# Performance work log

Measured on AMD Instinct MI355X. Metric: run time of the kernel, lower is better.

## Reference

```python
import jax, jax.numpy as jnp
import numpy as np

NUM_RELATIONS = 3
NUM_HEADS = 1

N_NODES = 50000
N_EDGES = 300000
D = 256  # in_channels == out_channels == out_channels*num_heads
W_SCALE = 0.02  # realistic init scale; keeps linear-attention normalizer dominated by N_r


def setup_inputs() -> dict:
    key = jax.random.key(0)
    k = jax.random.split(key, 7)
    x = jax.random.normal(k[0], (N_NODES, D), dtype=jnp.float32)
    Wq = jax.random.normal(k[1], (NUM_RELATIONS, D, D * NUM_HEADS), dtype=jnp.float32) * W_SCALE
    Wk = jax.random.normal(k[2], (NUM_RELATIONS, D, D * NUM_HEADS), dtype=jnp.float32) * W_SCALE
    Wv = jax.random.normal(k[3], (NUM_RELATIONS, D, D * NUM_HEADS), dtype=jnp.float32) * W_SCALE
    Whp = jax.random.normal(k[4], (D * NUM_HEADS, D), dtype=jnp.float32) * W_SCALE
    edge_index = jax.random.randint(k[5], (2, N_EDGES), 0, N_NODES, dtype=jnp.int64)
    edge_type = jax.random.randint(k[6], (N_EDGES,), 0, NUM_RELATIONS, dtype=jnp.int64)
    return {"x": x, "Wq": Wq, "Wk": Wk, "Wv": Wv, "Whp": Whp,
            "edge_index": edge_index, "edge_type": edge_type}


def _trans_conv(x, Wq, Wk, Wv, Whp, edge_index, edge_type):
    # x: [N, F], Wq/Wk/Wv: [R, F, H*Dh], Whp: [H*Dh, Dh], edge_index: [2, E]
    row, col = edge_index[0], edge_index[1]
    N = x.shape[0]
    R = Wq.shape[0]
    H = NUM_HEADS
    Dh = Wq.shape[-1] // H
    xr = x[row]  # [E, F] gathered source-node features
    xc = x[col]  # [E, F] gathered target-node features
    x_out = jnp.zeros((N, Dh), dtype=x.dtype)
    for r in range(R):  # small fixed relation loop (structurally distinct weights)
        m = (edge_type == r).astype(x.dtype)  # [E] relation mask (handles ragged sizes)
        Nr = jnp.sum(m)  # number of edges of this relation (the 'N' in full_attention_conv)
        q = (xr @ Wq[r]).reshape(-1, H, Dh)  # [E, H, Dh]
        kk = (xc @ Wk[r]).reshape(-1, H, Dh)
        v = (xc @ Wv[r]).reshape(-1, H, Dh)
        # linear attention (no softmax), masked so only relation-r edges contribute
        kvs = jnp.einsum('e,ehm,ehd->hmd', m, kk, v)        # [H, Dh, Dh]
        num = jnp.einsum('ehm,hmd->ehd', q, kvs) + Nr * v    # [E, H, Dh]
        ks_sum = jnp.einsum('e,ehm->hm', m, kk)              # [H, Dh]
        norm = jnp.einsum('ehm,hm->eh', q, ks_sum)[..., None] + Nr  # [E, H, 1]
        attn = (num / norm).mean(axis=1)                     # [E, Dh] (mean over heads)
        x_out = x_out.at[row].add(m[:, None] * attn)         # scatter-add to source nodes
    return x_out @ Whp  # head projection


def reference(x, Wq, Wk, Wv, Whp, edge_index, edge_type):
    return _trans_conv(x, Wq, Wk, Wv, Whp, edge_index, edge_type)
```

## Files before the change

### kernel.cpp

```cpp
#include <hip/hip_runtime.h>

#define NN 50000
#define EE 300000
#define DD 256
#define RR 3
#define NPAD 50048
#define GS 64
#define SCT (RR * NN)
#define SCB 1024
#define SNB ((SCT + SCB - 1) / SCB)
#define TBLK 3128
#define WBLK 2560
#define CBLK 512

using bf16x8 = __attribute__((ext_vector_type(8))) short;
using f32x4  = __attribute__((ext_vector_type(4))) float;

__device__ __forceinline__ float bf2f(unsigned short u) {
    return __uint_as_float(((unsigned)u) << 16);
}
__device__ __forceinline__ unsigned short f2bf(float f) {
    unsigned u = __float_as_uint(f);
    return (unsigned short)((u + 0x7fffu + ((u >> 16) & 1u)) >> 16);
}
__device__ __forceinline__ void gload_lds16(const void* g, void* l) {
    __builtin_amdgcn_global_load_lds(
        (const __attribute__((address_space(1))) unsigned int*)g,
        (__attribute__((address_space(3))) unsigned int*)l, 16, 0, 0);
}

__global__ __launch_bounds__(256) void prep_tc(
    const float* __restrict__ x, const float* __restrict__ Wq,
    const float* __restrict__ Wk, const float* __restrict__ Wv,
    const float* __restrict__ Whp,
    unsigned short* __restrict__ xb, unsigned short* __restrict__ xT,
    unsigned short* __restrict__ Wqb, unsigned short* __restrict__ Wkb,
    unsigned short* __restrict__ Wvb, unsigned short* __restrict__ WhpT,
    const int* __restrict__ erow, const int* __restrict__ ecol,
    const int* __restrict__ etype, int* __restrict__ c_in,
    int* __restrict__ c_out, int* __restrict__ nr)
{
    const int tid = threadIdx.x;
    if (blockIdx.x < TBLK) {
        __shared__ unsigned short t[64][66];
        const int tb = blockIdx.x;
        const int n0 = (tb % 782) * 64, i0 = (tb / 782) * 64;
        const int nl = tid >> 2, c0 = (tid & 3) * 16;
        unsigned short vb[16];
        int n = n0 + nl;
        if (n < NN) {
            const float* src = x + (size_t)n * DD + i0 + c0;
#pragma unroll
            for (int q = 0; q < 16; q += 4) {
                float4 v = *(const float4*)(src + q);
                vb[q] = f2bf(v.x); vb[q + 1] = f2bf(v.y);
                vb[q + 2] = f2bf(v.z); vb[q + 3] = f2bf(v.w);
            }
#pragma unroll
            for (int q = 0; q < 16; q += 4)
                *(ushort4*)(xb + (size_t)n * DD + i0 + c0 + q) =
                    make_ushort4(vb[q], vb[q + 1], vb[q + 2], vb[q + 3]);
        } else {
#pragma unroll
            for (int q = 0; q < 16; q++) vb[q] = 0;
        }
#pragma unroll
        for (int q = 0; q < 16; q++) t[nl][c0 + q] = vb[q];
        __syncthreads();
        const int il = tid >> 2, nc0 = (tid & 3) * 16;
        unsigned short ob[16];
#pragma unroll
        for (int q = 0; q < 16; q++) ob[q] = t[nc0 + q][il];
#pragma unroll
        for (int q = 0; q < 16; q += 4)
            *(ushort4*)(xT + (size_t)(i0 + il) * NPAD + n0 + nc0 + q) =
                make_ushort4(ob[q], ob[q + 1], ob[q + 2], ob[q + 3]);
    } else if (blockIdx.x < TBLK + WBLK) {
        int t = (blockIdx.x - TBLK) * 256 + tid;
        int slot = t >> 16, o = t & 65535;
        int a = o >> 8, b = o & 255;
        if (slot < 3)       Wqb[(size_t)slot * 65536 + o] = f2bf(Wq[(size_t)slot * 65536 + o]);
        else if (slot < 6)  Wkb[(size_t)(slot - 3) * 65536 + o] = f2bf(Wk[(size_t)(slot - 3) * 65536 + o]);
        else if (slot < 9)  Wvb[(size_t)(slot - 6) * 65536 + o] = f2bf(Wv[(size_t)(slot - 6) * 65536 + o]);
        else if (slot == 9) WhpT[o] = f2bf(Whp[b * 256 + a]);
    } else {
        __shared__ int lnr[RR];
        if (tid < RR) lnr[tid] = 0;
        __syncthreads();
        int cb = blockIdx.x - (TBLK + WBLK);
        for (int e = cb * 256 + tid; e < EE; e += CBLK * 256) {
            int t = etype[e];
            atomicAdd(&c_out[t * NN + erow[e]], 1);
            atomicAdd(&c_in[t * NN + ecol[e]], 1);
            atomicAdd(&lnr[t], 1);
        }
        __syncthreads();
        if (tid < RR) atomicAdd(&nr[tid], lnr[tid]);
    }
}

__global__ __launch_bounds__(256) void prep2(
    const int* __restrict__ c_out, int* __restrict__ bsum,
    const unsigned short* __restrict__ xT, const int* __restrict__ c_in,
    float* __restrict__ xw, unsigned short* __restrict__ wbf)
{
    const int tid = threadIdx.x;
    if (blockIdx.x < SNB) {
        __shared__ int ws[4];
        const int b = blockIdx.x;
        const int i = b * SCB + tid * 4;
        int s = 0;
        if (i < SCT) {
            int4 v = *(const int4*)(c_out + i);
            s = v.x + v.y + v.z + v.w;
        }
#pragma unroll
        for (int off = 32; off; off >>= 1) s += __shfl_down(s, off, 64);
        if ((tid & 63) == 0) ws[tid >> 6] = s;
        __syncthreads();
        if (tid == 0) bsum[b] = ws[0] + ws[1] + ws[2] + ws[3];
    } else if (blockIdx.x < SNB + 256) {
        __shared__ float red[3][4];
        const int i = blockIdx.x - SNB;
        float a0 = 0.f, a1 = 0.f, a2 = 0.f;
        for (int n = tid * 4; n < NN; n += 1024) {
            ushort4 xv = *(const ushort4*)(xT + (size_t)i * NPAD + n);
            int4 w0 = *(const int4*)(c_in + n);
            int4 w1 = *(const int4*)(c_in + NN + n);
            int4 w2 = *(const int4*)(c_in + 2 * NN + n);
            float f0 = bf2f(xv.x), f1 = bf2f(xv.y), f2 = bf2f(xv.z), f3 = bf2f(xv.w);
            a0 += f0 * w0.x + f1 * w0.y + f2 * w0.z + f3 * w0.w;
            a1 += f0 * w1.x + f1 * w1.y + f2 * w1.z + f3 * w1.w;
            a2 += f0 * w2.x + f1 * w2.y + f2 * w2.z + f3 * w2.w;
        }
#pragma unroll
        for (int off = 32; off; off >>= 1) {
            a0 += __shfl_down(a0, off, 64);
            a1 += __shfl_down(a1, off, 64);
            a2 += __shfl_down(a2, off, 64);
        }
        if ((tid & 63) == 0) {
            red[0][tid >> 6] = a0; red[1][tid >> 6] = a1; red[2][tid >> 6] = a2;
        }
        __syncthreads();
        if (tid < 3)
            xw[tid * 256 + i] = red[tid][0] + red[tid][1] + red[tid][2] + red[tid][3];
    } else {
        int t = (blockIdx.x - SNB - 256) * 256 + tid;
        if (t < 3 * NPAD) {
            int r = t / NPAD, n = t % NPAD;
            wbf[t] = f2bf(n < NN ? (float)c_in[r * NN + n] : 0.f);
        }
    }
}

__global__ __launch_bounds__(256) void scan_bot(
    const int* __restrict__ cnt, const int* __restrict__ bsum,
    int* __restrict__ off, int* __restrict__ cur)
{
    __shared__ int bs[256], loc[256];
    const int b = blockIdx.x, tid = threadIdx.x;
    int v = tid < SNB ? bsum[tid] : 0;
    bs[tid] = v;
    __syncthreads();
    for (int d = 1; d < 256; d <<= 1) {
        int t = (tid >= d) ? bs[tid - d] : 0;
        __syncthreads();
        bs[tid] += t;
        __syncthreads();
    }
    const int myboff = b ? bs[b - 1] : 0;
    const int total = bs[255];
    const int i = b * SCB + tid * 4;
    int4 vv = make_int4(0, 0, 0, 0);
    if (i < SCT) vv = *(const int4*)(cnt + i);
    int s = vv.x + vv.y + vv.z + vv.w;
    loc[tid] = s;
    __syncthreads();
    for (int d = 1; d < 256; d <<= 1) {
        int t = (tid >= d) ? loc[tid - d] : 0;
        __syncthreads();
        loc[tid] += t;
        __syncthreads();
    }
    if (i < SCT) {
        int pre = myboff + (tid ? loc[tid - 1] : 0);
        int4 o;
        o.x = pre;
        o.y = pre + vv.x;
        o.z = pre + vv.x + vv.y;
        o.w = pre + vv.x + vv.y + vv.z;
        *(int4*)(off + i) = o;
        *(int4*)(cur + i) = o;
    }
    if (b == 0 && tid == 0) off[SCT] = total;
}

__global__ __launch_bounds__(256) void fill_kernel(
    const int* __restrict__ erow, const int* __restrict__ ecol,
    const int* __restrict__ etype, int* __restrict__ cur,
    int* __restrict__ scol)
{
    int e = blockIdx.x * 256 + threadIdx.x;
    if (e < EE) {
        int key = etype[e] * NN + erow[e];
        int p = atomicAdd(&cur[key], 1);
        scol[p] = ecol[e];
    }
}

__global__ __launch_bounds__(512) void g_kernel(
    const unsigned short* __restrict__ xT, const unsigned short* __restrict__ wbf,
    float* __restrict__ Gp)
{
    __shared__ __align__(16) char ldsA[16384];
    __shared__ __align__(16) char ldsB[16384];
    const int tid = threadIdx.x, lane = tid & 63, wid = tid >> 6;
    const int wr = wid >> 1, wc = wid & 1;
    const int i0 = blockIdx.x * 128, j0 = blockIdx.y * 128;
    const int TPZ = (NPAD / 64 + GS - 1) / GS;
    const int kt0 = blockIdx.z * TPZ;
    const int kt1 = min(NPAD / 64, kt0 + TPZ);

    f32x4 acc[3][2][4];
#pragma unroll
    for (int r = 0; r < 3; r++)
#pragma unroll
        for (int m = 0; m < 2; m++)
#pragma unroll
            for (int n = 0; n < 4; n++) acc[r][m][n] = (f32x4){0.f, 0.f, 0.f, 0.f};

    for (int kt = kt0; kt < kt1; kt++) {
        const int kbyte = kt * 128;
#pragma unroll
        for (int is = 0; is < 2; is++) {
            int lb = is * 8192 + wid * 1024;
            int d = lb + lane * 16;
            int row = d >> 7;
            int sc_ = (d & 127) ^ ((row & 7) << 4);
            gload_lds16((const char*)xT + (size_t)(i0 + row) * (NPAD * 2) + kbyte + sc_, ldsA + lb);
            gload_lds16((const char*)xT + (size_t)(j0 + row) * (NPAD * 2) + kbyte + sc_, ldsB + lb);
        }
        __syncthreads();
#pragma unroll
        for (int kk = 0; kk < 2; kk++) {
            const int cb = kk * 64 + ((lane >> 4) << 4);
            bf16x8 bfr[4];
#pragma unroll
            for (int n = 0; n < 4; n++) {
                int rn = wc * 64 + n * 16 + (lane & 15);
                bfr[n] = *(const bf16x8*)(ldsB + rn * 128 + (cb ^ ((rn & 7) << 4)));
            }
            float au[2][8];
#pragma unroll
            for (int m = 0; m < 2; m++) {
                int row = wr * 32 + m * 16 + (lane & 15);
                bf16x8 ar = *(const bf16x8*)(ldsA + row * 128 + (cb ^ ((row & 7) << 4)));
#pragma unroll
                for (int q = 0; q < 8; q++) au[m][q] = bf2f((unsigned short)ar[q]);
            }
            const int nb = kt * 64 + kk * 32 + ((lane >> 4) << 3);
#pragma unroll
            for (int r = 0; r < 3; r++) {
                bf16x8 wv = *(const bf16x8*)(wbf + (size_t)r * NPAD + nb);
                float wf[8];
#pragma unroll
                for (int q = 0; q < 8; q++) wf[q] = bf2f((unsigned short)wv[q]);
                bf16x8 am[2];
#pragma unroll
                for (int m = 0; m < 2; m++)
#pragma unroll
                    for (int q = 0; q < 8; q++)
                        am[m][q] = (short)f2bf(au[m][q] * wf[q]);
#pragma unroll
                for (int m = 0; m < 2; m++)
#pragma unroll
                    for (int n = 0; n < 4; n++)
                        acc[r][m][n] = __builtin_amdgcn_mfma_f32_16x16x32_bf16(
                            am[m], bfr[n], acc[r][m][n], 0, 0, 0);
            }
        }
        __syncthreads();
    }
    float* base = Gp + ((size_t)blockIdx.z * 4 + blockIdx.x * 2 + blockIdx.y) * 3 * 16384;
#pragma unroll
    for (int r = 0; r < 3; r++)
#pragma unroll
        for (int m = 0; m < 2; m++)
#pragma unroll
            for (int n = 0; n < 4; n++) {
                int col = wc * 64 + n * 16 + (lane & 15);
                int rw0 = wr * 32 + m * 16 + ((lane >> 4) << 2);
#pragma unroll
                for (int reg = 0; reg < 4; reg++)
                    base[r * 16384 + (rw0 + reg) * 128 + col] = acc[r][m][n][reg];
            }
}

__global__ __launch_bounds__(256) void gred_mv(
    const float* __restrict__ Gp, unsigned short* __restrict__ Gb,
    const unsigned short* __restrict__ M1, const float* __restrict__ xw,
    float* __restrict__ tv)
{
    const int tid = threadIdx.x;
    if (blockIdx.x < 768) {
        int gid = blockIdx.x * 256 + tid;
        int t = gid >> 14, rem = gid & 16383;
        int r = t % 3, tile = t / 3;
        float s = 0.f;
        for (int z = 0; z < GS; z++)
            s += Gp[(size_t)z * 196608 + ((size_t)tile * 3 + r) * 16384 + rem];
        int i = (tile >> 1) * 128 + (rem >> 7);
        int j = (tile & 1) * 128 + (rem & 127);
        Gb[(size_t)r * 65536 + i * 256 + j] = f2bf(s);
    } else {
        __shared__ float vs[256];
        const int b = blockIdx.x - 768;
        const int r = b >> 6, rb = (b & 63) * 4;
        vs[tid] = xw[r * 256 + tid];
        __syncthreads();
        const int wid = tid >> 6, lane = tid & 63;
        const int row = rb + wid;
        ushort4 m4 = *(const ushort4*)(M1 + (size_t)r * 65536 + row * 256 + lane * 4);
        float s = bf2f(m4.x) * vs[lane * 4] + bf2f(m4.y) * vs[lane * 4 + 1] +
                  bf2f(m4.z) * vs[lane * 4 + 2] + bf2f(m4.w) * vs[lane * 4 + 3];
#pragma unroll
        for (int off = 32; off; off >>= 1) s += __shfl_down(s, off, 64);
        if (lane == 0) tv[r * 256 + row] = s;
    }
}

__global__ __launch_bounds__(256) void gather_kernel(
    const unsigned short* __restrict__ xb, const int* __restrict__ scol,
    const int* __restrict__ off, const float* __restrict__ tv,
    const int* __restrict__ c_out, const int* __restrict__ nr,
    unsigned short* __restrict__ Ascat, float* __restrict__ s2g)
{
    __shared__ float ts[768];
    __shared__ float nrs[RR];
    const int tid = threadIdx.x;
    for (int k = tid; k < 768; k += 256) ts[k] = tv[k];
    if (tid < RR) nrs[tid] = (float)nr[tid];
    __syncthreads();
    const int wid = tid >> 6, lane = tid & 63;
    const int n = blockIdx.x * 4 + wid;
    if (n >= NN) return;
    ushort4 xv = *(const ushort4*)(xb + (size_t)n * DD + lane * 4);
    float xf[4] = {bf2f(xv.x), bf2f(xv.y), bf2f(xv.z), bf2f(xv.w)};
    float dots[RR];
#pragma unroll
    for (int t = 0; t < RR; t++) {
        float s = xf[0] * ts[t * 256 + lane * 4] + xf[1] * ts[t * 256 + lane * 4 + 1] +
                  xf[2] * ts[t * 256 + lane * 4 + 2] + xf[3] * ts[t * 256 + lane * 4 + 3];
#pragma unroll
        for (int o = 32; o; o >>= 1) s += __shfl_xor(s, o, 64);
        dots[t] = s;
    }
    int i0 = off[0 * NN + n], e0 = off[0 * NN + n + 1];
    int i1 = off[1 * NN + n], e1 = off[1 * NN + n + 1];
    int i2 = off[2 * NN + n], e2 = off[2 * NN + n + 1];
    float a0[4] = {0.f, 0.f, 0.f, 0.f};
    float a1[4] = {0.f, 0.f, 0.f, 0.f};
    float a2[4] = {0.f, 0.f, 0.f, 0.f};
    while (i0 < e0 || i1 < e1 || i2 < e2) {
        bool h0 = i0 < e0, h1 = i1 < e1, h2 = i2 < e2;
        ushort4 v0, v1, v2;
        if (h0) { int c = scol[i0]; v0 = *(const ushort4*)(xb + (size_t)c * DD + lane * 4); }
        if (h1) { int c = scol[i1]; v1 = *(const ushort4*)(xb + (size_t)c * DD + lane * 4); }
        if (h2) { int c = scol[i2]; v2 = *(const ushort4*)(xb + (size_t)c * DD + lane * 4); }
        if (h0) { a0[0] += bf2f(v0.x); a0[1] += bf2f(v0.y);
                  a0[2] += bf2f(v0.z); a0[3] += bf2f(v0.w); i0++; }
        if (h1) { a1[0] += bf2f(v1.x); a1[1] += bf2f(v1.y);
                  a1[2] += bf2f(v1.z); a1[3] += bf2f(v1.w); i1++; }
        if (h2) { a2[0] += bf2f(v2.x); a2[1] += bf2f(v2.y);
                  a2[2] += bf2f(v2.z); a2[3] += bf2f(v2.w); i2++; }
    }
    float* accs[3] = {a0, a1, a2};
#pragma unroll
    for (int t = 0; t < RR; t++) {
        float nrf = nrs[t];
        float denom = dots[t] + nrf;
        if (lane == 0) {
            int cnt = c_out[t * NN + n];
            s2g[(size_t)t * NN + n] = cnt ? (float)cnt / denom : 0.f;
        }
        float s1 = nrf / denom;
        float* a = accs[t];
        ushort4 o2;
        o2.x = f2bf(s1 * a[0]); o2.y = f2bf(s1 * a[1]);
        o2.z = f2bf(s1 * a[2]); o2.w = f2bf(s1 * a[3]);
        *(ushort4*)(Ascat + (size_t)n * 768 + t * 256 + lane * 4) = o2;
    }
}

template <int MODE, int SWZ>
__global__ __launch_bounds__(256) void gemm_nt(
    const unsigned short* __restrict__ A, int lda,
    const unsigned short* __restrict__ B, int ldb,
    void* __restrict__ Cv, int ldc, int M, int KK,
    size_t sa, size_t sb, size_t sc)
{
    A += (size_t)blockIdx.z * sa;
    B += (size_t)blockIdx.z * sb;
    __shared__ __align__(16) char ldsA[16384];
    __shared__ __align__(16) char ldsB[16384];
    const int tid = threadIdx.x, lane = tid & 63, wid = tid >> 6;
    const int wr = wid >> 1, wc = wid & 1;
    int bx = blockIdx.x;
    if (SWZ) {
        int nwg = gridDim.x, q = nwg >> 3, rem = nwg & 7;
        int xcd = bx & 7, idx = bx >> 3;
        bx = (xcd < rem ? xcd * (q + 1) : rem * (q + 1) + (xcd - rem) * q) + idx;
    }
    const int row0 = bx * 128, col0 = blockIdx.y * 128;

    f32x4 acc[4][4];
#pragma unroll
    for (int m = 0; m < 4; m++)
#pragma unroll
        for (int n = 0; n < 4; n++) acc[m][n] = (f32x4){0.f, 0.f, 0.f, 0.f};

    for (int k0 = 0; k0 < KK; k0 += 64) {
#pragma unroll
        for (int is = 0; is < 4; is++) {
            int lb = is * 4096 + wid * 1024;
            int d = lb + lane * 16;
            int row = d >> 7;
            int sc_ = (d & 127) ^ ((row & 7) << 4);
            int gr = row0 + row; gr = gr < M ? gr : M - 1;
            gload_lds16((const char*)(A + (size_t)gr * lda + k0) + sc_, ldsA + lb);
            int rn = col0 + row;
            gload_lds16((const char*)(B + (size_t)rn * ldb + k0) + sc_, ldsB + lb);
        }
        __syncthreads();
#pragma unroll
        for (int kk = 0; kk < 2; kk++) {
            bf16x8 af[4], bf_[4];
            const int cb = kk * 64 + ((lane >> 4) << 4);
#pragma unroll
            for (int m = 0; m < 4; m++) {
                int row = wr * 64 + m * 16 + (lane & 15);
                af[m] = *(const bf16x8*)(ldsA + row * 128 + (cb ^ ((row & 7) << 4)));
                int rn = wc * 64 + m * 16 + (lane & 15);
                bf_[m] = *(const bf16x8*)(ldsB + rn * 128 + (cb ^ ((rn & 7) << 4)));
            }
#pragma unroll
            for (int m = 0; m < 4; m++)
#pragma unroll
                for (int n = 0; n < 4; n++)
                    acc[m][n] = __builtin_amdgcn_mfma_f32_16x16x32_bf16(
                        af[m], bf_[n], acc[m][n], 0, 0, 0);
        }
        __syncthreads();
    }

#pragma unroll
    for (int m = 0; m < 4; m++) {
#pragma unroll
        for (int reg = 0; reg < 4; reg++) {
            int r = row0 + wr * 64 + m * 16 + ((lane >> 4) << 2) + reg;
            if (r >= M) continue;
#pragma unroll
            for (int n = 0; n < 4; n++) {
                int c = col0 + wc * 64 + n * 16 + (lane & 15);
                float v = acc[m][n][reg];
                if (MODE == 0)
                    ((unsigned short*)Cv)[(size_t)blockIdx.z * sc + (size_t)r * ldc + c] = f2bf(v);
                else
                    ((float*)Cv)[(size_t)blockIdx.z * sc + (size_t)r * ldc + c] = v;
            }
        }
    }
}

__global__ __launch_bounds__(512) void gemm_big(
    const unsigned short* __restrict__ Xb, const unsigned short* __restrict__ As,
    const unsigned short* __restrict__ Bm, const float* __restrict__ s2g,
    float* __restrict__ C, int M)
{
    extern __shared__ __align__(16) char lds[];
    char* ldsA = lds;
    char* ldsB = lds + 32768;
    float* s2l = (float*)(lds + 98304);
    const int tid = threadIdx.x, lane = tid & 63, wid = tid >> 6;
    const int wr = wid >> 2, wc = wid & 3;
    int bx = blockIdx.x;
    {
        int nwg = gridDim.x, q = nwg >> 3, rem = nwg & 7;
        int xcd = bx & 7, idx = bx >> 3;
        bx = (xcd < rem ? xcd * (q + 1) : rem * (q + 1) + (xcd - rem) * q) + idx;
    }
    const int row0 = bx * 128;

    if (tid < 384) {
        int rsel = tid >> 7, rr = tid & 127;
        int gr = row0 + rr; gr = gr < M ? gr : M - 1;
        s2l[tid] = s2g[(size_t)rsel * NN + gr];
    }

    f32x4 accO[4][4], acc[4][4];
#pragma unroll
    for (int m = 0; m < 4; m++)
#pragma unroll
        for (int n = 0; n < 4; n++) {
            accO[m][n] = (f32x4){0.f, 0.f, 0.f, 0.f};
            acc[m][n]  = (f32x4){0.f, 0.f, 0.f, 0.f};
        }

#define STAGE_A(buf, Asrc, ldaE, kE)                                           \
    { _Pragma("unroll")                                                        \
      for (int is = 0; is < 2; is++) {                                         \
          int lb = is * 8192 + wid * 1024;                                     \
          int d = lb + lane * 16;                                              \
          int row = d >> 7;                                                    \
          int sc_ = (d & 127) ^ ((row & 7) << 4);                              \
          int gr = row0 + row; gr = gr < M ? gr : M - 1;                       \
          gload_lds16((const char*)((Asrc) + (size_t)gr * (ldaE) + (kE)) + sc_,\
                      ldsA + (buf) * 16384 + lb); } }

#define STAGE_B(buf, kE)                                                       \
    { _Pragma("unroll")                                                        \
      for (int is = 0; is < 4; is++) {                                         \
          int lb = is * 8192 + wid * 1024;                                     \
          int d = lb + lane * 16;                                              \
          int row = d >> 7;                                                    \
          int sc_ = (d & 127) ^ ((row & 7) << 4);                              \
          gload_lds16((const char*)(Bm + (size_t)row * 1536 + (kE)) + sc_,     \
                      ldsB + (buf) * 32768 + lb); } }

#define MFMA_STEP(abuf, bbuf, ACC)                                             \
    { const char* bA = ldsA + (abuf) * 16384;                                  \
      const char* bB = ldsB + (bbuf) * 32768;                                  \
      _Pragma("unroll")                                                        \
      for (int kk = 0; kk < 2; kk++) {                                         \
          bf16x8 af[4], bf_[4];                                                \
          const int cb = kk * 64 + ((lane >> 4) << 4);                         \
          _Pragma("unroll")                                                    \
          for (int m = 0; m < 4; m++) {                                        \
              int row = wr * 64 + m * 16 + (lane & 15);                        \
              af[m] = *(const bf16x8*)(bA + row * 128 + (cb ^ ((row & 7) << 4)));\
              int rn = wc * 64 + m * 16 + (lane & 15);                         \
              bf_[m] = *(const bf16x8*)(bB + rn * 128 + (cb ^ ((rn & 7) << 4)));\
          }                                                                    \
          _Pragma("unroll")                                                    \
          for (int m = 0; m < 4; m++)                                          \
              _Pragma("unroll")                                                \
              for (int n = 0; n < 4; n++)                                      \
                  ACC[m][n] = __builtin_amdgcn_mfma_f32_16x16x32_bf16(         \
                      af[m], bf_[n], ACC[m][n], 0, 0, 0); } }

    STAGE_A(0, Xb, 256, 0);
    STAGE_B(0, 0);
    __syncthreads();
    int ab = 0, bb = 0;

    for (int r = 0; r < 3; r++) {
        for (int kt = 0; kt < 4; kt++) {
            if (kt < 3)      { STAGE_A(ab ^ 1, Xb, 256, (kt + 1) * 64);
                               STAGE_B(bb ^ 1, r * 256 + (kt + 1) * 64); }
            else if (r < 2)  { STAGE_A(ab ^ 1, Xb, 256, 0);
                               STAGE_B(bb ^ 1, (r + 1) * 256); }
            else             { STAGE_A(ab ^ 1, As, 768, 0);
                               STAGE_B(bb ^ 1, 768); }
            MFMA_STEP(ab, bb, acc);
            __syncthreads();
            ab ^= 1; bb ^= 1;
        }
#pragma unroll
        for (int m = 0; m < 4; m++) {
            f32x4 sv = *(const f32x4*)&s2l[r * 128 + wr * 64 + m * 16 + ((lane >> 4) << 2)];
#pragma unroll
            for (int n = 0; n < 4; n++) {
                accO[m][n] += sv * acc[m][n];
                acc[m][n] = (f32x4){0.f, 0.f, 0.f, 0.f};
            }
        }
    }
    for (int st = 0; st < 12; st++) {
        if (st < 11) { STAGE_A(ab ^ 1, As, 768, (st + 1) * 64);
                       STAGE_B(bb ^ 1, 768 + (st + 1) * 64); }
        MFMA_STEP(ab, bb, accO);
        __syncthreads();
        ab ^= 1; bb ^= 1;
    }
#undef STAGE_A
#undef STAGE_B
#undef MFMA_STEP

#pragma unroll
    for (int m = 0; m < 4; m++) {
#pragma unroll
        for (int reg = 0; reg < 4; reg++) {
            int r = row0 + wr * 64 + m * 16 + ((lane >> 4) << 2) + reg;
            if (r >= M) continue;
#pragma unroll
            for (int n = 0; n < 4; n++) {
                int c = wc * 64 + n * 16 + (lane & 15);
                C[(size_t)r * 256 + c] = accO[m][n][reg];
            }
        }
    }
}

extern "C" void kernel_launch(void* const* d_in, const int* in_sizes, int n_in,
                              void* d_out, int out_size, void* d_ws, size_t ws_size,
                              hipStream_t stream)
{
    const float* x   = (const float*)d_in[0];
    const float* Wq  = (const float*)d_in[1];
    const float* Wk  = (const float*)d_in[2];
    const float* Wv  = (const float*)d_in[3];
    const float* Whp = (const float*)d_in[4];
    const int* eidx  = (const int*)d_in[5];
    const int* etyp  = (const int*)d_in[6];
    const int* erow = eidx;
    const int* ecol = eidx + EE;
    float* out = (float*)d_out;

    char* p = (char*)d_ws;
    unsigned short* xb    = (unsigned short*)p; p += (size_t)NN * DD * 2;
    unsigned short* xT    = (unsigned short*)p; p += (size_t)DD * NPAD * 2;
    char*           regB  = p;                  p += (size_t)NN * 768 * 2;
    unsigned short* Gb    = (unsigned short*)p; p += (size_t)RR * 65536 * 2;
    unsigned short* M1    = (unsigned short*)p; p += (size_t)RR * 65536 * 2;
    unsigned short* Tm    = (unsigned short*)p; p += (size_t)RR * 65536 * 2;
    unsigned short* Bout  = (unsigned short*)p; p += (size_t)256 * 1536 * 2;
    unsigned short* Wqb   = (unsigned short*)p; p += (size_t)RR * 65536 * 2;
    unsigned short* Wkb   = (unsigned short*)p; p += (size_t)RR * 65536 * 2;
    unsigned short* Wvb   = (unsigned short*)p; p += (size_t)RR * 65536 * 2;
    unsigned short* WhpT  = (unsigned short*)p; p += 65536 * 2;
    unsigned short* wbf   = (unsigned short*)p; p += (size_t)RR * NPAD * 2;
    float*          xw    = (float*)p;          p += 768 * 4;
    float*          tv    = (float*)p;          p += 768 * 4;
    float*          s2g   = (float*)p;          p += (size_t)RR * NN * 4;
    int*            c_in  = (int*)p;            p += (size_t)RR * NN * 4;
    int*            c_out = (int*)p;            p += (size_t)RR * NN * 4;
    int*            nr    = (int*)p;            p += 4 * 4;
    int*            off   = (int*)p;            p += (size_t)(RR * NN + 4) * 4;
    int*            cur   = (int*)p;            p += (size_t)RR * NN * 4;
    int*            scol  = (int*)p;            p += (size_t)EE * 4;
    int*            bsum  = (int*)p;            p += SNB * 4;
    float*          Gp    = (float*)regB;
    unsigned short* Ascat = (unsigned short*)regB;

    hipFuncSetAttribute((const void*)gemm_big,
                        hipFuncAttributeMaxDynamicSharedMemorySize, 99840);

    hipMemsetAsync(c_in, 0, (size_t)(6 * NN + 4) * sizeof(int), stream);
    prep_tc<<<TBLK + WBLK + CBLK, 256, 0, stream>>>(
        x, Wq, Wk, Wv, Whp, xb, xT, Wqb, Wkb, Wvb, WhpT,
        erow, ecol, etyp, c_in, c_out, nr);
    prep2<<<SNB + 256 + (3 * NPAD + 255) / 256, 256, 0, stream>>>(
        c_out, bsum, xT, c_in, xw, wbf);
    scan_bot<<<SNB, 256, 0, stream>>>(c_out, bsum, off, cur);
    fill_kernel<<<(EE + 255) / 256, 256, 0, stream>>>(erow, ecol, etyp, cur, scol);

    gemm_nt<0, 0><<<dim3(2, 2, 3), 256, 0, stream>>>(Wqb, 256, Wkb, 256, M1, 256, 256, 256,
                                                     65536, 65536, 65536);
    gemm_nt<0, 0><<<dim3(2, 2, 3), 256, 0, stream>>>(WhpT, 256, Wvb, 256, Bout + 768, 1536,
                                                     256, 256, 0, 65536, 256);

    g_kernel<<<dim3(2, 2, GS), 512, 0, stream>>>(xT, wbf, Gp);
    gred_mv<<<768 + 192, 256, 0, stream>>>(Gp, Gb, M1, xw, tv);

    gemm_nt<0, 0><<<dim3(2, 2, 3), 256, 0, stream>>>(M1, 256, Gb, 256, Tm, 256, 256, 256,
                                                     65536, 65536, 65536);
    gemm_nt<0, 0><<<dim3(2, 2, 3), 256, 0, stream>>>(Bout + 768, 1536, Tm, 256, Bout, 1536,
                                                     256, 256, 256, 65536, 256);

    gather_kernel<<<(NN + 3) / 4, 256, 0, stream>>>(
        xb, scol, off, tv, c_out, nr, Ascat, s2g);

    const int MB2 = (NN + 127) / 128;
    gemm_big<<<dim3(MB2, 1), 512, 99840, stream>>>(xb, Ascat, Bout, s2g, out, NN);
}
```

Measured before the change: 289.3 us.

## Triple-buffer gemm_big LDS with two-stage-ahead async loads and vmcnt waits

Rewrites the final fused GEMM's main loop as a single 24-step pipeline with three LDS buffers. Loads run two stages ahead and are synchronized through explicit s_waitcnt vmcnt(6) plus a raw barrier instead of __syncthreads. The aim is to hide global-to-LDS latency behind MFMA work. In exchange, LDS use per block grows to about 149KB, which limits occupancy to one block per CU, and the hand-written waitcnt logic risks races if the counts are wrong.

```diff
diff --git a/kernel.cpp b/kernel.cpp
--- a/kernel.cpp
+++ b/kernel.cpp
@@ -480,8 +480,8 @@
 {
     extern __shared__ __align__(16) char lds[];
     char* ldsA = lds;
-    char* ldsB = lds + 32768;
-    float* s2l = (float*)(lds + 98304);
+    char* ldsB = lds + 49152;
+    float* s2l = (float*)(lds + 147456);
     const int tid = threadIdx.x, lane = tid & 63, wid = tid >> 6;
     const int wr = wid >> 2, wc = wid & 3;
     int bx = blockIdx.x;
@@ -507,30 +507,36 @@
             acc[m][n]  = (f32x4){0.f, 0.f, 0.f, 0.f};
         }
 
-#define STAGE_A(buf, Asrc, ldaE, kE)                                           \
-    { _Pragma("unroll")                                                        \
-      for (int is = 0; is < 2; is++) {                                         \
-          int lb = is * 8192 + wid * 1024;                                     \
-          int d = lb + lane * 16;                                              \
-          int row = d >> 7;                                                    \
-          int sc_ = (d & 127) ^ ((row & 7) << 4);                              \
-          int gr = row0 + row; gr = gr < M ? gr : M - 1;                       \
-          gload_lds16((const char*)((Asrc) + (size_t)gr * (ldaE) + (kE)) + sc_,\
-                      ldsA + (buf) * 16384 + lb); } }
-
-#define STAGE_B(buf, kE)                                                       \
-    { _Pragma("unroll")                                                        \
-      for (int is = 0; is < 4; is++) {                                         \
-          int lb = is * 8192 + wid * 1024;                                     \
-          int d = lb + lane * 16;                                              \
-          int row = d >> 7;                                                    \
-          int sc_ = (d & 127) ^ ((row & 7) << 4);                              \
-          gload_lds16((const char*)(Bm + (size_t)row * 1536 + (kE)) + sc_,     \
-                      ldsB + (buf) * 32768 + lb); } }
-
-#define MFMA_STEP(abuf, bbuf, ACC)                                             \
-    { const char* bA = ldsA + (abuf) * 16384;                                  \
-      const char* bB = ldsB + (bbuf) * 32768;                                  \
+#define STAGE(buf, j)                                                          \
+    {                                                                          \
+        const unsigned short* Asrc_ = (j) < 12 ? Xb : As;                      \
+        const int ldaE_ = (j) < 12 ? 256 : 768;                                \
+        const int kA_ = (j) < 12 ? ((j) & 3) * 64 : ((j) - 12) * 64;           \
+        const int kB_ = (j) * 64;                                              \
+        _Pragma("unroll")                                                      \
+        for (int is = 0; is < 2; is++) {                                       \
+            int lb = is * 8192 + wid * 1024;                                   \
+            int d = lb + lane * 16;                                            \
+            int row = d >> 7;                                                  \
+            int sc_ = (d & 127) ^ ((row & 7) << 4);                            \
+            int gr = row0 + row; gr = gr < M ? gr : M - 1;                     \
+            gload_lds16((const char*)(Asrc_ + (size_t)gr * ldaE_ + kA_) + sc_, \
+                        ldsA + (buf) * 16384 + lb);                            \
+        }                                                                      \
+        _Pragma("unroll")                                                      \
+        for (int is = 0; is < 4; is++) {                                       \
+            int lb = is * 8192 + wid * 1024;                                   \
+            int d = lb + lane * 16;                                            \
+            int row = d >> 7;                                                  \
+            int sc_ = (d & 127) ^ ((row & 7) << 4);                            \
+            gload_lds16((const char*)(Bm + (size_t)row * 1536 + kB_) + sc_,    \
+                        ldsB + (buf) * 32768 + lb);                            \
+        }                                                                      \
+    }
+
+#define MFMA_STEP(buf, ACC)                                                    \
+    { const char* bA = ldsA + (buf) * 16384;                                   \
+      const char* bB = ldsB + (buf) * 32768;                                   \
       _Pragma("unroll")                                                        \
       for (int kk = 0; kk < 2; kk++) {                                         \
           bf16x8 af[4], bf_[4];                                                \
@@ -549,42 +555,34 @@
                   ACC[m][n] = __builtin_amdgcn_mfma_f32_16x16x32_bf16(         \
                       af[m], bf_[n], ACC[m][n], 0, 0, 0); } }
 
-    STAGE_A(0, Xb, 256, 0);
-    STAGE_B(0, 0);
-    __syncthreads();
-    int ab = 0, bb = 0;
-
-    for (int r = 0; r < 3; r++) {
-        for (int kt = 0; kt < 4; kt++) {
-            if (kt < 3)      { STAGE_A(ab ^ 1, Xb, 256, (kt + 1) * 64);
-                               STAGE_B(bb ^ 1, r * 256 + (kt + 1) * 64); }
-            else if (r < 2)  { STAGE_A(ab ^ 1, Xb, 256, 0);
-                               STAGE_B(bb ^ 1, (r + 1) * 256); }
-            else             { STAGE_A(ab ^ 1, As, 768, 0);
-                               STAGE_B(bb ^ 1, 768); }
-            MFMA_STEP(ab, bb, acc);
-            __syncthreads();
-            ab ^= 1; bb ^= 1;
-        }
-#pragma unroll
-        for (int m = 0; m < 4; m++) {
-            f32x4 sv = *(const f32x4*)&s2l[r * 128 + wr * 64 + m * 16 + ((lane >> 4) << 2)];
-#pragma unroll
-            for (int n = 0; n < 4; n++) {
-                accO[m][n] += sv * acc[m][n];
-                acc[m][n] = (f32x4){0.f, 0.f, 0.f, 0.f};
-            }
-        }
-    }
-    for (int st = 0; st < 12; st++) {
-        if (st < 11) { STAGE_A(ab ^ 1, As, 768, (st + 1) * 64);
-                       STAGE_B(bb ^ 1, 768 + (st + 1) * 64); }
-        MFMA_STEP(ab, bb, accO);
-        __syncthreads();
-        ab ^= 1; bb ^= 1;
-    }
-#undef STAGE_A
-#undef STAGE_B
+    STAGE(0, 0);
+    STAGE(1, 1);
+    asm volatile("s_waitcnt vmcnt(6) lgkmcnt(0)" ::: "memory");
+    __builtin_amdgcn_s_barrier();
+    asm volatile("" ::: "memory");
+
+    for (int t = 0; t < 24; t++) {
+        if (t + 2 < 24) STAGE((t + 2) % 3, t + 2);
+        if (t < 12) { MFMA_STEP(t % 3, acc); }
+        else        { MFMA_STEP(t % 3, accO); }
+        if (t < 22) asm volatile("s_waitcnt vmcnt(6)" ::: "memory");
+        else        asm volatile("s_waitcnt vmcnt(0)" ::: "memory");
+        __builtin_amdgcn_s_barrier();
+        asm volatile("" ::: "memory");
+        if (t < 12 && (t & 3) == 3) {
+            int pp = t >> 2;
+#pragma unroll
+            for (int m = 0; m < 4; m++) {
+                f32x4 sv = *(const f32x4*)&s2l[pp * 128 + wr * 64 + m * 16 + ((lane >> 4) << 2)];
+#pragma unroll
+                for (int n = 0; n < 4; n++) {
+                    accO[m][n] += sv * acc[m][n];
+                    acc[m][n] = (f32x4){0.f, 0.f, 0.f, 0.f};
+                }
+            }
+        }
+    }
+#undef STAGE
 #undef MFMA_STEP
 
 #pragma unroll
@@ -644,7 +642,7 @@
     unsigned short* Ascat = (unsigned short*)regB;
 
     hipFuncSetAttribute((const void*)gemm_big,
-                        hipFuncAttributeMaxDynamicSharedMemorySize, 99840);
+                        hipFuncAttributeMaxDynamicSharedMemorySize, 148992);
 
     hipMemsetAsync(c_in, 0, (size_t)(6 * NN + 4) * sizeof(int), stream);
     prep_tc<<<TBLK + WBLK + CBLK, 256, 0, stream>>>(
@@ -672,5 +670,5 @@
         xb, scol, off, tv, c_out, nr, Ascat, s2g);
 
     const int MB2 = (NN + 127) / 128;
-    gemm_big<<<dim3(MB2, 1), 512, 99840, stream>>>(xb, Ascat, Bout, s2g, out, NN);
-}
+    gemm_big<<<dim3(MB2, 1), 512, 148992, stream>>>(xb, Ascat, Bout, s2g, out, NN);
+}
```

Result: slower. 345.2 us (+19.4%).
